# Kernel tuning notes

Measured on AMD Instinct MI355X. Metric: run time of the kernel, lower is better.

## Reference

```python
import jax, jax.numpy as jnp
import numpy as np

B, T, F = 16, 2000, 1024

# SA neuron constants (defaults from __init__)
I_TAU = 2.5e-11
I_TH = 8.3e-09
I_TAU_AHP = 2e-11
I_TH_AHP = 1.66e-11
I_TAU_REF = 1.6e-09
C_MEM = 1e-13
C_ADAP = 2.5e-13
C_REF = 2e-13
U_T = 0.026
KAPPA = 0.7
A_FRAC = 0.8
Z_RESET = 0.0
I_IN_OP = 5e-10
CURRENT_SCALE = 1e-12

TAU_S = C_MEM * U_T / max(KAPPA * I_TAU, 1e-30)
DT_MS = max(1e-06, TAU_S * 1000.0 / 20.0)
DT_S = DT_MS * 0.001
R = I_TH / max(I_TAU, 1e-30)
Z_TH = I_IN_OP / max(1.0 - A_FRAC, 1e-12)
ONE_MINUS_A = max(1.0 - A_FRAC, 1e-12)
TAU_M = max(C_MEM * U_T / max(KAPPA * I_TAU, 1e-30), 1e-12)
TAU_AHP = max(C_ADAP * U_T / max(KAPPA * I_TAU_AHP, 1e-30), 1e-12)
TAU_REF = max(C_REF * U_T / max(KAPPA * I_TAU_REF, 1e-30), 1e-12)


def setup_inputs() -> dict:
    key = jax.random.key(0)
    input_current = jax.random.normal(key, (B, T, F), dtype=jnp.float32)
    return {"input_current": input_current}


def _sa_forward(input_current):
    b, t, f = input_current.shape
    dtype = input_current.dtype
    x = jnp.swapaxes(input_current, 0, 1)  # [T,B,F] for scan

    dt_s = jnp.asarray(DT_S, dtype)
    z_th = jnp.asarray(Z_TH, dtype)
    z_reset = jnp.asarray(Z_RESET, dtype)
    i_th_ahp = jnp.asarray(I_TH_AHP, dtype)
    i_tau_ref = jnp.asarray(I_TAU_REF, dtype)

    def step(carry, i_in_t):
        z, i_ahp, i_ref = carry
        i_in = i_in_t * CURRENT_SCALE
        i_net = i_in - i_ahp - i_ref
        dz_dt = (-(ONE_MINUS_A * z) + i_net) / TAU_M
        z_next = z + dt_s * dz_dt
        fired = z_next >= z_th
        z_next = jnp.where(fired, z_reset, z_next)
        i_ahp_next = i_ahp + dt_s * (-(i_ahp / TAU_AHP))
        i_ref_next = i_ref + dt_s * (-(i_ref / TAU_REF))
        i_ahp_next = jnp.where(fired, i_ahp_next + i_th_ahp, i_ahp_next)
        i_ref_next = jnp.where(fired, i_ref_next + i_tau_ref, i_ref_next)
        return (z_next, i_ahp_next, i_ref_next), (z_next * R, fired)

    z0 = jnp.zeros((b, f), dtype)
    init = (z0, jnp.zeros((b, f), dtype), jnp.zeros((b, f), dtype))
    _, (imem_steps, fired_steps) = jax.lax.scan(step, init, x)  # [T,B,F]

    # imem_trace[:,0,:] = 0 (z0 * r); then per-step membrane currents
    imem_trace = jnp.concatenate(
        [jnp.zeros((1, b, f), dtype), imem_steps], axis=0
    )
    imem_trace = jnp.swapaxes(imem_trace, 0, 1)  # [B,T+1,F]

    # spikes[:,t,:] = fired_t for t<T; spikes[:,T,:] = fired_{T-1}
    # (each step writes t and t+1; the t+1 write is overwritten except the last)
    spikes = jnp.concatenate([fired_steps, fired_steps[-1:]], axis=0)
    spikes = jnp.swapaxes(spikes, 0, 1)  # [B,T+1,F] bool
    return imem_trace, spikes


def reference(input_current):
    return _sa_forward(input_current)
```

## Files before the change

kernel.cpp:

```cpp
#include <hip/hip_runtime.h>


namespace {
constexpr int Bb = 16;
constexpr int Tt = 2000;
constexpr int Ff = 1024;
constexpr int CH = 10;
constexpr int Lc = Tt / CH;
constexpr int TS = 25;
constexpr int OT = Lc / TS;
constexpr int HALO = 500;

constexpr float AZ  = 0.99f;
constexpr float KIN = 1.66e-11f;
constexpr float CAHP = 0.984f;
constexpr float KA  = 2.7556e-10f;
constexpr float CREF = -0.6f;
constexpr float KR  = 2.656e-8f;
constexpr float YTH = 8.3e-7f;
}

__global__ __launch_bounds__(64, 2) void sa_scan(const float* __restrict__ in,
                                                 float* __restrict__ out) {
  const int lane = threadIdx.x;
  const int blk  = blockIdx.x;
  const int c    = blk >> 8;
  const int g    = blk & 255;
  const int b    = g >> 4;
  const int f0   = (g & 15) << 6;

  const float* gx = in + (size_t)b * Tt * Ff + f0 + lane;

  const int t_out = c * Lc;
  const int t_h   = (t_out > HALO) ? t_out - HALO : 0;
  const int nh    = (t_out - t_h) / TS;

  float* imem_p = out + ((size_t)b * (Tt + 1) + t_out + 1) * Ff + f0 + lane;
  float* spk_p =
      out + ((size_t)(Bb + b)) * (size_t)(Tt + 1) * Ff + (size_t)t_out * Ff +
      f0 + lane;

  if (c == 0) __builtin_nontemporal_store(0.0f, imem_p - Ff);

  float A[TS], B[TS];
  float y = 0.0f, iA = 0.0f, iR = 0.0f, lastspk = 0.0f;

#define LOADT(buf, ti)                                        \
  {                                                           \
    const float* p = gx + (size_t)(t_h + (ti) * TS) * Ff;     \
    _Pragma("unroll") for (int j = 0; j < TS; ++j)            \
        buf[j] = p[(size_t)j * Ff];                           \
  }

#define HSTEP(xval)                                  \
  {                                                  \
    float x = (xval);                                \
    float inet = fmaf(x, KIN, -(iA + iR));           \
    y = fmaf(y, AZ, inet);                           \
    bool fired = y >= YTH;                           \
    y = fired ? 0.0f : y;                            \
    iA = fmaf(iA, CAHP, fired ? KA : 0.0f);          \
    iR = fmaf(iR, CREF, fired ? KR : 0.0f);          \
  }

#define FSTEP(xval)                                  \
  {                                                  \
    float x = (xval);                                \
    float inet = fmaf(x, KIN, -(iA + iR));           \
    y = fmaf(y, AZ, inet);                           \
    bool fired = y >= YTH;                           \
    y = fired ? 0.0f : y;                            \
    lastspk = fired ? 1.0f : 0.0f;                   \
    iA = fmaf(iA, CAHP, fired ? KA : 0.0f);          \
    iR = fmaf(iR, CREF, fired ? KR : 0.0f);          \
    __builtin_nontemporal_store(y, imem_p);          \
    __builtin_nontemporal_store(lastspk, spk_p);     \
    imem_p += Ff;                                    \
    spk_p += Ff;                                     \
  }

  LOADT(A, 0);

  for (int i = 0; i < nh; i += 2) {
    LOADT(B, i + 1);
#pragma unroll
    for (int j = 0; j < TS; ++j) HSTEP(A[j]);
    LOADT(A, i + 2);
#pragma unroll
    for (int j = 0; j < TS; ++j) HSTEP(B[j]);
  }

  for (int i = nh; i < nh + OT; i += 2) {
    LOADT(B, i + 1);
#pragma unroll
    for (int j = 0; j < TS; ++j) FSTEP(A[j]);
    if (i + 2 < nh + OT) LOADT(A, i + 2);
#pragma unroll
    for (int j = 0; j < TS; ++j) FSTEP(B[j]);
  }

  if (c == CH - 1) __builtin_nontemporal_store(lastspk, spk_p);

#undef LOADT
#undef HSTEP
#undef FSTEP
}

extern "C" void kernel_launch(void* const* d_in, const int* in_sizes, int n_in,
                              void* d_out, int out_size, void* d_ws,
                              size_t ws_size, hipStream_t stream) {
  const float* in = (const float*)d_in[0];
  float* out = (float*)d_out;
  dim3 grid(CH * Bb * (Ff / 64));
  dim3 block(64);
  hipLaunchKernelGGL(sa_scan, grid, block, 0, stream, in, out);
}
```

Before: 87.74 us.

## Vectorize scan to four features per lane with float4 I/O and more time chunks

Each lane now runs four independent neuron recurrences and uses 16-byte vector loads and nontemporal stores instead of scalar ones. To keep the grid size up, the time axis is split into 20 chunks instead of 10, each still warmed up over a 500-step halo, and the load tile shrinks to 10 steps. The aim is more instruction-level parallelism per thread and wider memory transactions. In exchange, the grid goes from 2560 to 1280 blocks, redundant halo work per output step doubles relative to chunk length, and register pressure rises with the four sets of state and the vector buffers.

```diff
diff --git a/kernel.cpp b/kernel.cpp
--- a/kernel.cpp
+++ b/kernel.cpp
@@ -2,12 +2,15 @@
 
 
 namespace {
+typedef float f32x4 __attribute__((ext_vector_type(4)));
+
 constexpr int Bb = 16;
 constexpr int Tt = 2000;
 constexpr int Ff = 1024;
-constexpr int CH = 10;
+constexpr int F4 = Ff / 4;
+constexpr int CH = 20;
 constexpr int Lc = Tt / CH;
-constexpr int TS = 25;
+constexpr int TS = 10;
 constexpr int OT = Lc / TS;
 constexpr int HALO = 500;
 
@@ -24,59 +27,68 @@
                                                  float* __restrict__ out) {
   const int lane = threadIdx.x;
   const int blk  = blockIdx.x;
-  const int c    = blk >> 8;
-  const int g    = blk & 255;
-  const int b    = g >> 4;
-  const int f0   = (g & 15) << 6;
+  const int c    = blk >> 6;
+  const int g    = blk & 63;
+  const int b    = g >> 2;
+  const int f    = ((g & 3) << 8) + (lane << 2);
 
-  const float* gx = in + (size_t)b * Tt * Ff + f0 + lane;
+  const f32x4* gx = (const f32x4*)(in + (size_t)b * Tt * Ff + f);
 
   const int t_out = c * Lc;
   const int t_h   = (t_out > HALO) ? t_out - HALO : 0;
   const int nh    = (t_out - t_h) / TS;
 
-  float* imem_p = out + ((size_t)b * (Tt + 1) + t_out + 1) * Ff + f0 + lane;
-  float* spk_p =
-      out + ((size_t)(Bb + b)) * (size_t)(Tt + 1) * Ff + (size_t)t_out * Ff +
-      f0 + lane;
+  f32x4* imem_p = (f32x4*)(out + ((size_t)b * (Tt + 1) + t_out + 1) * Ff + f);
+  f32x4* spk_p =
+      (f32x4*)(out + ((size_t)(Bb + b) * (Tt + 1) + t_out) * Ff + f);
 
-  if (c == 0) __builtin_nontemporal_store(0.0f, imem_p - Ff);
-
-  float A[TS], B[TS];
-  float y = 0.0f, iA = 0.0f, iR = 0.0f, lastspk = 0.0f;
-
-#define LOADT(buf, ti)                                        \
-  {                                                           \
-    const float* p = gx + (size_t)(t_h + (ti) * TS) * Ff;     \
-    _Pragma("unroll") for (int j = 0; j < TS; ++j)            \
-        buf[j] = p[(size_t)j * Ff];                           \
+  if (c == 0) {
+    f32x4 zz = {0.0f, 0.0f, 0.0f, 0.0f};
+    __builtin_nontemporal_store(zz, imem_p - F4);
   }
 
-#define HSTEP(xval)                                  \
-  {                                                  \
-    float x = (xval);                                \
-    float inet = fmaf(x, KIN, -(iA + iR));           \
-    y = fmaf(y, AZ, inet);                           \
-    bool fired = y >= YTH;                           \
-    y = fired ? 0.0f : y;                            \
-    iA = fmaf(iA, CAHP, fired ? KA : 0.0f);          \
-    iR = fmaf(iR, CREF, fired ? KR : 0.0f);          \
+  f32x4 A[TS], B[TS];
+  float y0 = 0, y1 = 0, y2 = 0, y3 = 0;
+  float a0 = 0, a1 = 0, a2 = 0, a3 = 0;
+  float r0 = 0, r1 = 0, r2 = 0, r3 = 0;
+  float s0 = 0, s1 = 0, s2 = 0, s3 = 0;
+
+#define LOADT(buf, ti)                                     \
+  {                                                        \
+    const f32x4* p = gx + (size_t)(t_h + (ti) * TS) * F4;  \
+    _Pragma("unroll") for (int j = 0; j < TS; ++j)         \
+        buf[j] = p[(size_t)j * F4];                        \
   }
 
-#define FSTEP(xval)                                  \
-  {                                                  \
-    float x = (xval);                                \
-    float inet = fmaf(x, KIN, -(iA + iR));           \
-    y = fmaf(y, AZ, inet);                           \
-    bool fired = y >= YTH;                           \
-    y = fired ? 0.0f : y;                            \
-    lastspk = fired ? 1.0f : 0.0f;                   \
-    iA = fmaf(iA, CAHP, fired ? KA : 0.0f);          \
-    iR = fmaf(iR, CREF, fired ? KR : 0.0f);          \
-    __builtin_nontemporal_store(y, imem_p);          \
-    __builtin_nontemporal_store(lastspk, spk_p);     \
-    imem_p += Ff;                                    \
-    spk_p += Ff;                                     \
+#define CSTEP(x, y, a, r, s)                       \
+  {                                                \
+    float inet = fmaf((x), KIN, -((a) + (r)));     \
+    (y) = fmaf((y), AZ, inet);                     \
+    bool fd = (y) >= YTH;                          \
+    (y) = fd ? 0.0f : (y);                         \
+    (s) = fd ? 1.0f : 0.0f;                        \
+    (a) = fmaf((a), CAHP, fd ? KA : 0.0f);         \
+    (r) = fmaf((r), CREF, fd ? KR : 0.0f);         \
+  }
+
+#define HSTEP(xv)                  \
+  {                                \
+    f32x4 x_ = (xv);               \
+    CSTEP(x_[0], y0, a0, r0, s0);  \
+    CSTEP(x_[1], y1, a1, r1, s1);  \
+    CSTEP(x_[2], y2, a2, r2, s2);  \
+    CSTEP(x_[3], y3, a3, r3, s3);  \
+  }
+
+#define FSTEP(xv)                                  \
+  {                                                \
+    HSTEP(xv);                                     \
+    f32x4 yo = {y0, y1, y2, y3};                   \
+    f32x4 so = {s0, s1, s2, s3};                   \
+    __builtin_nontemporal_store(yo, imem_p);       \
+    __builtin_nontemporal_store(so, spk_p);        \
+    imem_p += F4;                                  \
+    spk_p += F4;                                   \
   }
 
   LOADT(A, 0);
@@ -99,9 +111,13 @@
     for (int j = 0; j < TS; ++j) FSTEP(B[j]);
   }
 
-  if (c == CH - 1) __builtin_nontemporal_store(lastspk, spk_p);
+  if (c == CH - 1) {
+    f32x4 so = {s0, s1, s2, s3};
+    __builtin_nontemporal_store(so, spk_p);
+  }
 
 #undef LOADT
+#undef CSTEP
 #undef HSTEP
 #undef FSTEP
 }
@@ -111,7 +127,7 @@
                               size_t ws_size, hipStream_t stream) {
   const float* in = (const float*)d_in[0];
   float* out = (float*)d_out;
-  dim3 grid(CH * Bb * (Ff / 64));
+  dim3 grid(CH * Bb * (Ff / 256));
   dim3 block(64);
   hipLaunchKernelGGL(sa_scan, grid, block, 0, stream, in, out);
 }
```

Measured after the change: 117.1 us. 33.4% more time.
